# Optimization experiments

Measured on AMD Instinct MI355X. Metric: run time of the kernel, lower is better.

Reference implementation:

```python
import jax, jax.numpy as jnp
import numpy as np

B, Y = 1024, 50000
MAX_TRIALS = 4096


def setup_inputs() -> dict:
    key = jax.random.key(0)
    k1, k2 = jax.random.split(key)
    input_ = jax.random.normal(k1, (B, Y), dtype=jnp.float32)
    pos = jax.random.randint(k2, (B,), 0, Y)
    target = jnp.zeros((B, Y), jnp.float32).at[jnp.arange(B), pos].set(1.0)
    return {"input_": input_, "target": target, "max_num_trials": MAX_TRIALS}


def reference(input_, target, max_num_trials):
    """WARP loss. The torch original sequentially samples negatives WITHOUT
    replacement per row until margin 1 + s_neg - s_pos >= 0 or max_num_trials
    is hit. Sampling without replacement == taking a uniform random
    permutation of the negative labels and scanning it; the first violating
    position t gives num_trials = t+1. This lets us fully vectorize the
    irregular loop while computing identical math (up to RNG stream)."""
    Bn, Yn = input_.shape
    rows = jnp.arange(Bn)
    pos = jnp.argmax(target, axis=1)                 # one positive per row (as J[i,1])
    pos_score = input_[rows, pos]                    # [B]

    # uniform random permutation of the Y-1 negatives per row:
    # random sort keys, force the positive label to sort last, drop it.
    u = jax.random.uniform(jax.random.key(42), (Bn, Yn))
    u = u.at[rows, pos].set(2.0)
    perm = jnp.argsort(u, axis=1)[:, : Yn - 1]       # [B, Y-1] negative label ids

    neg_scores = jnp.take_along_axis(input_, perm, axis=1)   # [B, Y-1]
    margins = 1.0 + neg_scores - pos_score[:, None]
    trial_ok = jnp.arange(Yn - 1)[None, :] < max_num_trials
    viol = (margins >= 0.0) & trial_ok
    found = jnp.any(viol, axis=1)
    first = jnp.argmax(viol, axis=1)                 # first violating trial index
    num_trials = (first + 1).astype(jnp.float32)
    # loss_weight = log(floor((Y-1)/num_trials)); 0 when no violator found
    L = jnp.where(found, jnp.log(jnp.floor((Yn - 1.0) / num_trials)), 0.0)
    neg_score = jnp.where(
        found, jnp.take_along_axis(neg_scores, first[:, None], axis=1)[:, 0], 0.0
    )
    loss = L * (1.0 - pos_score + neg_score)         # [B]
    return jnp.sum(loss, keepdims=True)              # shape (1,), as torch.sum(dim=0, keepdim=True)
```

## Files before the change

kernel.cpp:

```cpp
#include <hip/hip_runtime.h>
#include <stdint.h>

#define BN 1024
#define YN 50000
#define SEGS 8
#define SEGLEN 6250
#define CAP 192

#define TF_ROUND(r) { x0 += x1; x1 = (x1 << (r)) | (x1 >> (32 - (r))); x1 ^= x0; }

__device__ __forceinline__ uint32_t tf_bits(uint32_t ctr) {
    const uint32_t ks0 = 0u;
    const uint32_t ks1 = 42u;
    const uint32_t ks2 = 0x1BD11BDAu ^ 0u ^ 42u;
    uint32_t x1 = ctr + ks1;
    uint32_t x0 = x1;
    x1 = ((x1 << 13) | (x1 >> 19)) ^ x0;
    TF_ROUND(15) TF_ROUND(26) TF_ROUND(6)
    x0 += ks1; x1 += ks2 + 1u;
    TF_ROUND(17) TF_ROUND(29) TF_ROUND(16) TF_ROUND(24)
    x0 += ks2; x1 += ks0 + 2u;
    TF_ROUND(13) TF_ROUND(15) TF_ROUND(26) TF_ROUND(6)
    x0 += ks0; x1 += ks1 + 3u;
    TF_ROUND(17) TF_ROUND(29) TF_ROUND(16) TF_ROUND(24)
    x0 += ks1; x1 += ks2 + 4u;
    TF_ROUND(13) TF_ROUND(15) TF_ROUND(26) TF_ROUND(6)
    x0 += ks2; x1 += ks0 + 5u;
    return x0 ^ x1;
}

struct WS {
    uint32_t* cnt; uint32_t* done; int* pos; float* ps; float* row_loss; uint32_t* cand;
};
static inline WS ws_layout(void* d_ws) {
    uint32_t* p = (uint32_t*)d_ws;
    WS w;
    w.cnt = p; w.done = p + BN; w.pos = (int*)(p + 2 * BN);
    w.ps = (float*)(p + 3 * BN); w.row_loss = (float*)(p + 4 * BN);
    w.cand = p + 5 * BN;
    return w;
}

__global__ __launch_bounds__(256) void gen_kernel(
    const float* __restrict__ input, const float* __restrict__ target,
    uint32_t* __restrict__ cnt, uint32_t* __restrict__ cand,
    int* __restrict__ pos_out, float* __restrict__ ps_out)
{
    const int tid = threadIdx.x;
    if (blockIdx.x < BN) {
        const int row = blockIdx.x;
        const size_t base = (size_t)row * YN;
        __shared__ volatile int s_pos;
        if (tid == 0) s_pos = -1;
        __syncthreads();
        const float4* t4 = (const float4*)(target + base);
        for (int j4 = tid; j4 < YN / 4; j4 += 256) {
            if (s_pos >= 0) break;
            float4 v = t4[j4];
            int c0 = 4 * j4;
            if (v.x != 0.0f) s_pos = c0;
            if (v.y != 0.0f) s_pos = c0 + 1;
            if (v.z != 0.0f) s_pos = c0 + 2;
            if (v.w != 0.0f) s_pos = c0 + 3;
        }
        __syncthreads();
        if (tid == 0) {
            int p = s_pos;
            pos_out[row] = p;
            ps_out[row] = input[base + p];
        }
        return;
    }
    const int b = blockIdx.x - BN;
    const int row = b >> 3;
    const int seg = b & 7;
    const uint32_t base32 = (uint32_t)row * YN;
    const int start = seg * SEGLEN;
    const int end = start + SEGLEN;
    uint32_t* mycnt = cnt + row;
    uint32_t* mycand = cand + row * CAP;
    int col = start + tid;
    uint32_t ctr = base32 + (uint32_t)col;
    for (; col + 256 < end; col += 512, ctr += 512u) {
        uint32_t bits0 = tf_bits(ctr);
        uint32_t bits1 = tf_bits(ctr + 256u);
        if (bits0 < (1u << 23)) {
            uint32_t idx = atomicAdd(mycnt, 1u);
            if (idx < CAP) mycand[idx] = ((bits0 >> 9) << 17) | (uint32_t)col;
        }
        if (bits1 < (1u << 23)) {
            uint32_t idx = atomicAdd(mycnt, 1u);
            if (idx < CAP) mycand[idx] = ((bits1 >> 9) << 17) | (uint32_t)(col + 256);
        }
    }
    if (col < end) {
        uint32_t bits = tf_bits(ctr);
        if (bits < (1u << 23)) {
            uint32_t idx = atomicAdd(mycnt, 1u);
            if (idx < CAP) mycand[idx] = ((bits >> 9) << 17) | (uint32_t)col;
        }
    }
}

__global__ __launch_bounds__(256) void finish_kernel(
    const float* __restrict__ input, const uint32_t* __restrict__ cnt,
    const uint32_t* __restrict__ cand, const int* __restrict__ pos_,
    const float* __restrict__ ps_, const int* __restrict__ mt_ptr,
    float* __restrict__ row_loss, uint32_t* __restrict__ done,
    float* __restrict__ out)
{
    const int tid = threadIdx.x;
    const int lane = tid & 63;
    const int row = blockIdx.x * 4 + (tid >> 6);
    const int pos = pos_[row];
    const float ps = ps_[row];
    const float* rowp = input + (size_t)row * YN;
    const uint32_t n = cnt[row];
    const uint32_t mt = (uint32_t)mt_ptr[0];
    float loss = 0.0f;
    bool need_fallback = (n > CAP);

    if (!need_fallback) {
        const uint32_t* cl = cand + row * CAP;
        uint32_t mk = 0xFFFFFFFFu;
        for (uint32_t i = lane; i < n; i += 64) {
            uint32_t e = cl[i];
            int col = (int)(e & 0x1FFFFu);
            if (col != pos) {
                float s = rowp[col];
                if ((1.0f + s) - ps >= 0.0f) mk = (e < mk) ? e : mk;
            }
        }
        for (int off = 32; off > 0; off >>= 1) {
            uint32_t o = (uint32_t)__shfl_xor((int)mk, off, 64);
            mk = (o < mk) ? o : mk;
        }
        if (mk == 0xFFFFFFFFu) {
            need_fallback = true;
        } else {
            uint32_t c = 0;
            for (uint32_t i = lane; i < n; i += 64) {
                uint32_t e = cl[i];
                int col = (int)(e & 0x1FFFFu);
                c += ((e < mk) && (col != pos)) ? 1u : 0u;
            }
            for (int off = 32; off > 0; off >>= 1)
                c += (uint32_t)__shfl_xor((int)c, off, 64);
            if (c < mt) {
                int cstar = (int)(mk & 0x1FFFFu);
                float ns = rowp[cstar];
                float nt = (float)(c + 1u);
                loss = logf(floorf(49999.0f / nt)) * ((1.0f - ps) + ns);
            }
        }
    }
    if (need_fallback) {
        const uint32_t base32 = (uint32_t)row * YN;
        uint64_t mk = ~0ull;
        for (int col = lane; col < YN; col += 64) {
            uint32_t bits = tf_bits(base32 + (uint32_t)col);
            uint64_t key = ((uint64_t)(bits >> 9) << 17) | (uint32_t)col;
            float m = (1.0f + rowp[col]) - ps;
            if ((m >= 0.0f) && (col != pos) && (key < mk)) mk = key;
        }
        for (int off = 32; off > 0; off >>= 1) {
            uint64_t o = (uint64_t)__shfl_xor((long long)mk, off, 64);
            mk = (o < mk) ? o : mk;
        }
        if (mk != ~0ull) {
            uint32_t c = 0;
            for (int col = lane; col < YN; col += 64) {
                uint32_t bits = tf_bits(base32 + (uint32_t)col);
                uint64_t key = ((uint64_t)(bits >> 9) << 17) | (uint32_t)col;
                c += ((key < mk) && (col != pos)) ? 1u : 0u;
            }
            for (int off = 32; off > 0; off >>= 1)
                c += (uint32_t)__shfl_xor((int)c, off, 64);
            if (c < mt) {
                int cstar = (int)(mk & 0x1FFFFull);
                float ns = rowp[cstar];
                float nt = (float)(c + 1u);
                loss = logf(floorf(49999.0f / nt)) * ((1.0f - ps) + ns);
            }
        }
    }
    if (lane == 0) row_loss[row] = loss;

    __threadfence();
    __syncthreads();
    __shared__ bool s_last;
    if (tid == 0) s_last = (atomicAdd(done, 1u) == (uint32_t)(gridDim.x - 1));
    __syncthreads();
    if (s_last) {
        __threadfence();
        __shared__ float s[256];
        float acc = 0.0f;
        for (int i = tid; i < BN; i += 256) acc += row_loss[i];
        s[tid] = acc;
        __syncthreads();
        for (int st = 128; st > 0; st >>= 1) {
            if (tid < st) s[tid] += s[tid + st];
            __syncthreads();
        }
        if (tid == 0) out[0] = s[0];
    }
}

extern "C" void kernel_launch(void* const* d_in, const int* in_sizes, int n_in,
                              void* d_out, int out_size, void* d_ws, size_t ws_size,
                              hipStream_t stream) {
    const float* input  = (const float*)d_in[0];
    const float* target = (const float*)d_in[1];
    const int*   mt     = (const int*)d_in[2];
    float* out = (float*)d_out;
    WS w = ws_layout(d_ws);

    hipMemsetAsync(d_ws, 0, 2 * BN * sizeof(uint32_t), stream);

    gen_kernel<<<BN + BN * SEGS, 256, 0, stream>>>(
        input, target, w.cnt, w.cand, w.pos, w.ps);
    finish_kernel<<<BN / 4, 256, 0, stream>>>(
        input, w.cnt, w.cand, w.pos, w.ps, mt, w.row_loss, w.done, out);
}
```

Baseline: 470.7 us.

## Raise candidate threshold, parallelize fallback across block, and streamline Threefry with alignbit

The candidate threshold rises from 2^23 to 2^25 with a cap of 1024 when the workspace is large enough, so fewer rows miss a violator among the sampled candidates and fall back to a full 50000-column rescan. The fallback path now uses the whole 256-thread block per fallback row instead of a single wavefront, with shared-memory reductions. The Threefry hash is simplified: constant key terms are folded, rotations map to the alignbit builtin, and the generation loop is unrolled by four. The key packing changes from 17 to 16 column bits. Columns go up to 49999, which needs 16 bits, so the packing still fits, but the wider threshold means more atomics and candidate writes during generation.

```diff
diff --git a/kernel.cpp b/kernel.cpp
--- a/kernel.cpp
+++ b/kernel.cpp
@@ -5,27 +5,35 @@
 #define YN 50000
 #define SEGS 8
 #define SEGLEN 6250
-#define CAP 192
-
-#define TF_ROUND(r) { x0 += x1; x1 = (x1 << (r)) | (x1 >> (32 - (r))); x1 ^= x0; }
-
-__device__ __forceinline__ uint32_t tf_bits(uint32_t ctr) {
-    const uint32_t ks0 = 0u;
+#define CAP_BIG 1024
+#define CAP_SMALL 192
+
+#if defined(__has_builtin)
+#  if __has_builtin(__builtin_amdgcn_alignbit)
+#    define ROTL(x, r) __builtin_amdgcn_alignbit((x), (x), 32u - (r))
+#  endif
+#endif
+#ifndef ROTL
+#  define ROTL(x, r) (((x) << (r)) | ((x) >> (32 - (r))))
+#endif
+
+#define TFR(r) { x0 += x1; x1 = ROTL(x1, r) ^ x0; }
+
+__device__ __forceinline__ uint32_t tf_core(uint32_t v) {
     const uint32_t ks1 = 42u;
-    const uint32_t ks2 = 0x1BD11BDAu ^ 0u ^ 42u;
-    uint32_t x1 = ctr + ks1;
-    uint32_t x0 = x1;
-    x1 = ((x1 << 13) | (x1 >> 19)) ^ x0;
-    TF_ROUND(15) TF_ROUND(26) TF_ROUND(6)
+    const uint32_t ks2 = 0x1BD11BDAu ^ 42u;
+    uint32_t x0 = v;
+    uint32_t x1 = (ROTL(v, 13u)) ^ v;
+    TFR(15u) TFR(26u) TFR(6u)
     x0 += ks1; x1 += ks2 + 1u;
-    TF_ROUND(17) TF_ROUND(29) TF_ROUND(16) TF_ROUND(24)
-    x0 += ks2; x1 += ks0 + 2u;
-    TF_ROUND(13) TF_ROUND(15) TF_ROUND(26) TF_ROUND(6)
-    x0 += ks0; x1 += ks1 + 3u;
-    TF_ROUND(17) TF_ROUND(29) TF_ROUND(16) TF_ROUND(24)
+    TFR(17u) TFR(29u) TFR(16u) TFR(24u)
+    x0 += ks2; x1 += 2u;
+    TFR(13u) TFR(15u) TFR(26u) TFR(6u)
+     x1 += ks1 + 3u;
+    TFR(17u) TFR(29u) TFR(16u) TFR(24u)
     x0 += ks1; x1 += ks2 + 4u;
-    TF_ROUND(13) TF_ROUND(15) TF_ROUND(26) TF_ROUND(6)
-    x0 += ks2; x1 += ks0 + 5u;
+    TFR(13u) TFR(15u) TFR(26u) TFR(6u)
+    x0 += ks2; x1 += 5u;
     return x0 ^ x1;
 }
 
@@ -41,10 +49,18 @@
     return w;
 }
 
+__device__ __forceinline__ void push_cand(
+    uint32_t* mycnt, uint32_t* mycand, int cap, uint32_t bits, int col)
+{
+    uint32_t idx = atomicAdd(mycnt, 1u);
+    if (idx < (uint32_t)cap) mycand[idx] = ((bits >> 9) << 16) | (uint32_t)col;
+}
+
 __global__ __launch_bounds__(256) void gen_kernel(
     const float* __restrict__ input, const float* __restrict__ target,
     uint32_t* __restrict__ cnt, uint32_t* __restrict__ cand,
-    int* __restrict__ pos_out, float* __restrict__ ps_out)
+    int* __restrict__ pos_out, float* __restrict__ ps_out,
+    uint32_t thr, int cap)
 {
     const int tid = threadIdx.x;
     if (blockIdx.x < BN) {
@@ -76,29 +92,24 @@
     const int seg = b & 7;
     const uint32_t base32 = (uint32_t)row * YN;
     const int start = seg * SEGLEN;
-    const int end = start + SEGLEN;
     uint32_t* mycnt = cnt + row;
-    uint32_t* mycand = cand + row * CAP;
+    uint32_t* mycand = cand + (size_t)row * (size_t)cap;
     int col = start + tid;
-    uint32_t ctr = base32 + (uint32_t)col;
-    for (; col + 256 < end; col += 512, ctr += 512u) {
-        uint32_t bits0 = tf_bits(ctr);
-        uint32_t bits1 = tf_bits(ctr + 256u);
-        if (bits0 < (1u << 23)) {
-            uint32_t idx = atomicAdd(mycnt, 1u);
-            if (idx < CAP) mycand[idx] = ((bits0 >> 9) << 17) | (uint32_t)col;
-        }
-        if (bits1 < (1u << 23)) {
-            uint32_t idx = atomicAdd(mycnt, 1u);
-            if (idx < CAP) mycand[idx] = ((bits1 >> 9) << 17) | (uint32_t)(col + 256);
-        }
-    }
-    if (col < end) {
-        uint32_t bits = tf_bits(ctr);
-        if (bits < (1u << 23)) {
-            uint32_t idx = atomicAdd(mycnt, 1u);
-            if (idx < CAP) mycand[idx] = ((bits >> 9) << 17) | (uint32_t)col;
-        }
+    uint32_t cb = base32 + (uint32_t)col;
+    for (int k = 0; k < 6; ++k) {
+        uint32_t b0 = tf_core(cb + 42u);
+        uint32_t b1 = tf_core(cb + 298u);
+        uint32_t b2 = tf_core(cb + 554u);
+        uint32_t b3 = tf_core(cb + 810u);
+        if (b0 < thr) push_cand(mycnt, mycand, cap, b0, col);
+        if (b1 < thr) push_cand(mycnt, mycand, cap, b1, col + 256);
+        if (b2 < thr) push_cand(mycnt, mycand, cap, b2, col + 512);
+        if (b3 < thr) push_cand(mycnt, mycand, cap, b3, col + 768);
+        col += 1024; cb += 1024u;
+    }
+    if (tid < SEGLEN - 6144) {
+        uint32_t bt = tf_core(cb + 42u);
+        if (bt < thr) push_cand(mycnt, mycand, cap, bt, col);
     }
 }
 
@@ -107,25 +118,31 @@
     const uint32_t* __restrict__ cand, const int* __restrict__ pos_,
     const float* __restrict__ ps_, const int* __restrict__ mt_ptr,
     float* __restrict__ row_loss, uint32_t* __restrict__ done,
-    float* __restrict__ out)
+    float* __restrict__ out, int cap)
 {
     const int tid = threadIdx.x;
+    const int wid = tid >> 6;
     const int lane = tid & 63;
-    const int row = blockIdx.x * 4 + (tid >> 6);
+    const int row = blockIdx.x * 4 + wid;
     const int pos = pos_[row];
     const float ps = ps_[row];
     const float* rowp = input + (size_t)row * YN;
     const uint32_t n = cnt[row];
     const uint32_t mt = (uint32_t)mt_ptr[0];
+
+    __shared__ int s_fb[4];
+    __shared__ uint64_t s_min64[256];
+    __shared__ uint32_t s_sum[256];
+
     float loss = 0.0f;
-    bool need_fallback = (n > CAP);
+    bool need_fallback = (n > (uint32_t)cap);
 
     if (!need_fallback) {
-        const uint32_t* cl = cand + row * CAP;
+        const uint32_t* cl = cand + (size_t)row * (size_t)cap;
         uint32_t mk = 0xFFFFFFFFu;
         for (uint32_t i = lane; i < n; i += 64) {
             uint32_t e = cl[i];
-            int col = (int)(e & 0x1FFFFu);
+            int col = (int)(e & 0xFFFFu);
             if (col != pos) {
                 float s = rowp[col];
                 if ((1.0f + s) - ps >= 0.0f) mk = (e < mk) ? e : mk;
@@ -141,50 +158,76 @@
             uint32_t c = 0;
             for (uint32_t i = lane; i < n; i += 64) {
                 uint32_t e = cl[i];
-                int col = (int)(e & 0x1FFFFu);
+                int col = (int)(e & 0xFFFFu);
                 c += ((e < mk) && (col != pos)) ? 1u : 0u;
             }
             for (int off = 32; off > 0; off >>= 1)
                 c += (uint32_t)__shfl_xor((int)c, off, 64);
             if (c < mt) {
-                int cstar = (int)(mk & 0x1FFFFu);
+                int cstar = (int)(mk & 0xFFFFu);
                 float ns = rowp[cstar];
                 float nt = (float)(c + 1u);
                 loss = logf(floorf(49999.0f / nt)) * ((1.0f - ps) + ns);
             }
         }
     }
-    if (need_fallback) {
-        const uint32_t base32 = (uint32_t)row * YN;
-        uint64_t mk = ~0ull;
-        for (int col = lane; col < YN; col += 64) {
-            uint32_t bits = tf_bits(base32 + (uint32_t)col);
-            uint64_t key = ((uint64_t)(bits >> 9) << 17) | (uint32_t)col;
-            float m = (1.0f + rowp[col]) - ps;
-            if ((m >= 0.0f) && (col != pos) && (key < mk)) mk = key;
-        }
-        for (int off = 32; off > 0; off >>= 1) {
-            uint64_t o = (uint64_t)__shfl_xor((long long)mk, off, 64);
-            mk = (o < mk) ? o : mk;
-        }
-        if (mk != ~0ull) {
-            uint32_t c = 0;
-            for (int col = lane; col < YN; col += 64) {
-                uint32_t bits = tf_bits(base32 + (uint32_t)col);
-                uint64_t key = ((uint64_t)(bits >> 9) << 17) | (uint32_t)col;
-                c += ((key < mk) && (col != pos)) ? 1u : 0u;
-            }
-            for (int off = 32; off > 0; off >>= 1)
-                c += (uint32_t)__shfl_xor((int)c, off, 64);
-            if (c < mt) {
-                int cstar = (int)(mk & 0x1FFFFull);
-                float ns = rowp[cstar];
-                float nt = (float)(c + 1u);
-                loss = logf(floorf(49999.0f / nt)) * ((1.0f - ps) + ns);
-            }
-        }
-    }
-    if (lane == 0) row_loss[row] = loss;
+    if (lane == 0) {
+        s_fb[wid] = need_fallback ? row : -1;
+        if (!need_fallback) row_loss[row] = loss;
+    }
+    __syncthreads();
+
+    for (int w = 0; w < 4; ++w) {
+        const int frow = s_fb[w];
+        if (frow < 0) continue;
+        const int fpos = pos_[frow];
+        const float fps = ps_[frow];
+        const float* frp = input + (size_t)frow * YN;
+        const uint32_t fb32 = (uint32_t)frow * YN;
+        uint64_t mk64 = ~0ull;
+        for (int col = tid; col < YN; col += 256) {
+            uint32_t bits = tf_core(fb32 + (uint32_t)col + 42u);
+            uint64_t key = ((uint64_t)(bits >> 9) << 16) | (uint32_t)col;
+            float m = (1.0f + frp[col]) - fps;
+            if ((m >= 0.0f) && (col != fpos) && (key < mk64)) mk64 = key;
+        }
+        s_min64[tid] = mk64;
+        __syncthreads();
+        for (int s = 128; s > 0; s >>= 1) {
+            if (tid < s) { uint64_t o = s_min64[tid + s]; if (o < s_min64[tid]) s_min64[tid] = o; }
+            __syncthreads();
+        }
+        const uint64_t kstar = s_min64[0];
+        __syncthreads();
+        if (kstar == ~0ull) {
+            if (tid == 0) row_loss[frow] = 0.0f;
+            continue;
+        }
+        uint32_t c = 0;
+        for (int col = tid; col < YN; col += 256) {
+            uint32_t bits = tf_core(fb32 + (uint32_t)col + 42u);
+            uint64_t key = ((uint64_t)(bits >> 9) << 16) | (uint32_t)col;
+            c += ((key < kstar) && (col != fpos)) ? 1u : 0u;
+        }
+        s_sum[tid] = c;
+        __syncthreads();
+        for (int s = 128; s > 0; s >>= 1) {
+            if (tid < s) s_sum[tid] += s_sum[tid + s];
+            __syncthreads();
+        }
+        if (tid == 0) {
+            uint32_t rank = s_sum[0];
+            float fl = 0.0f;
+            if (rank < mt) {
+                int cstar = (int)(kstar & 0xFFFFull);
+                float ns = frp[cstar];
+                float nt = (float)(rank + 1u);
+                fl = logf(floorf(49999.0f / nt)) * ((1.0f - fps) + ns);
+            }
+            row_loss[frow] = fl;
+        }
+        __syncthreads();
+    }
 
     __threadfence();
     __syncthreads();
@@ -215,10 +258,15 @@
     float* out = (float*)d_out;
     WS w = ws_layout(d_ws);
 
+    const size_t need_big = (size_t)(5 * BN) * 4 + (size_t)BN * CAP_BIG * 4;
+    uint32_t thr; int cap;
+    if (ws_size >= need_big) { thr = 1u << 25; cap = CAP_BIG; }
+    else                     { thr = 1u << 23; cap = CAP_SMALL; }
+
     hipMemsetAsync(d_ws, 0, 2 * BN * sizeof(uint32_t), stream);
 
     gen_kernel<<<BN + BN * SEGS, 256, 0, stream>>>(
-        input, target, w.cnt, w.cand, w.pos, w.ps);
+        input, target, w.cnt, w.cand, w.pos, w.ps, thr, cap);
     finish_kernel<<<BN / 4, 256, 0, stream>>>(
-        input, w.cnt, w.cand, w.pos, w.ps, mt, w.row_loss, w.done, out);
-}
+        input, w.cnt, w.cand, w.pos, w.ps, mt, w.row_loss, w.done, out, cap);
+}
```

New measurement: 636.2 us. +35.2%, slower.
